# Kernel tuning notes

Hardware: AMD Instinct MI355X
Metric: run time of the kernel (lower is better)

Reference implementation:

```python
import jax, jax.numpy as jnp
import numpy as np

NUM_NODES = 50000
NUM_EDGES = 800000
HIDDEN = 128
HEADS = 8
HEAD_DIM = HIDDEN // HEADS  # 16
FF_HIDDEN = 4 * HIDDEN
LN_EPS = 1e-5


def _xavier(key, shape, gain=0.01):
    fan_out, fan_in = shape
    bound = gain * np.sqrt(6.0 / (fan_in + fan_out))
    return jax.random.uniform(key, shape, jnp.float32, -bound, bound)


def setup_inputs() -> dict:
    key = jax.random.key(0)
    ks = jax.random.split(key, 10)
    x = jax.random.normal(ks[0], (NUM_NODES, HIDDEN), jnp.float32)
    edge_index = jax.random.randint(ks[1], (2, NUM_EDGES), 0, NUM_NODES, jnp.int64)
    return {
        "x": x,
        "edge_index": edge_index,
        "Wq": _xavier(ks[2], (HIDDEN, HIDDEN)),
        "bq": jnp.zeros((HIDDEN,), jnp.float32),
        "Wk": _xavier(ks[3], (HIDDEN, HIDDEN)),
        "bk": jnp.zeros((HIDDEN,), jnp.float32),
        "Wv": _xavier(ks[4], (HIDDEN, HIDDEN)),
        "bv": jnp.zeros((HIDDEN,), jnp.float32),
        "Wo": _xavier(ks[5], (HIDDEN, HIDDEN)),
        "bo": jnp.zeros((HIDDEN,), jnp.float32),
        "W1": _xavier(ks[6], (FF_HIDDEN, HIDDEN)),
        "b1": jnp.zeros((FF_HIDDEN,), jnp.float32),
        "W2": _xavier(ks[7], (HIDDEN, FF_HIDDEN)),
        "b2": jnp.zeros((HIDDEN,), jnp.float32),
        "g1": jnp.ones((HIDDEN,), jnp.float32),
        "be1": jnp.zeros((HIDDEN,), jnp.float32),
        "g2": jnp.ones((HIDDEN,), jnp.float32),
        "be2": jnp.zeros((HIDDEN,), jnp.float32),
    }


def _layernorm(v, g, b):
    mu = jnp.mean(v, axis=-1, keepdims=True)
    var = jnp.mean(jnp.square(v - mu), axis=-1, keepdims=True)
    return (v - mu) * jax.lax.rsqrt(var + LN_EPS) * g + b


def _forward(x, edge_index, Wq, bq, Wk, bk, Wv, bv, Wo, bo, W1, b1, W2, b2, g1, be1, g2, be2):
    src = edge_index[0]  # key/value side (_j)
    dst = edge_index[1]  # query side (_i), aggregation index
    scale = 1.0 / np.sqrt(HEAD_DIM)

    # Euclidean manifold: GeometricLinear == plain linear
    q = (x @ Wq.T + bq).reshape(NUM_NODES, HEADS, HEAD_DIM)
    k = (x @ Wk.T + bk).reshape(NUM_NODES, HEADS, HEAD_DIM)
    v = (x @ Wv.T + bv).reshape(NUM_NODES, HEADS, HEAD_DIM)

    # per-edge attention scores [E, H]
    alpha = jnp.einsum('ehd,ehd->eh', q[dst], k[src]) * scale
    # segment softmax over destination nodes
    m = jax.ops.segment_max(alpha, dst, num_segments=NUM_NODES)  # [N, H]
    ea = jnp.exp(alpha - m[dst])
    denom = jax.ops.segment_sum(ea, dst, num_segments=NUM_NODES)  # [N, H]
    alpha = ea / (denom[dst] + 1e-16)

    # scatter-add weighted values -> [N, H, D]
    agg = jax.ops.segment_sum(v[src] * alpha[..., None], dst, num_segments=NUM_NODES)
    att = agg.reshape(NUM_NODES, HIDDEN) @ Wo.T + bo

    # residual + norm1 (Euclidean)
    h = _layernorm(x + att, g1, be1)

    # feed-forward: fc1 -> exact GELU -> fc2
    ff = (jax.nn.gelu(h @ W1.T + b1, approximate=False)) @ W2.T + b2

    # residual + norm2
    return _layernorm(h + ff, g2, be2)


def reference(x, edge_index, Wq, bq, Wk, bk, Wv, bv, Wo, bo, W1, b1, W2, b2, g1, be1, g2, be2):
    return _forward(x, edge_index, Wq, bq, Wk, bk, Wv, bv, Wo, bo, W1, b1, W2, b2, g1, be1, g2, be2)
```

## Files before the change

### kernel.cpp

```cpp
#include <hip/hip_runtime.h>
#include <math.h>

#define N_HEADS 8
#define HEAD_DIM 16
#define HID 128
#define QKV_ROWB 512

typedef unsigned short ushort_t;
typedef __attribute__((ext_vector_type(8))) short short8;
typedef __attribute__((ext_vector_type(4))) float floatx4;
typedef __attribute__((ext_vector_type(2))) float f32x2;

#define KV_SCALE 64.0f
#define KV_INV_SCALE 0.015625f

__device__ __forceinline__ ushort_t f2bf(float f) {
    unsigned u = __float_as_uint(f);
    unsigned r = (u + 0x7FFFu + ((u >> 16) & 1u)) >> 16;
    return (ushort_t)r;
}
__device__ __forceinline__ float bf2f(ushort_t u) {
    return __uint_as_float(((unsigned)u) << 16);
}

__device__ __forceinline__ void gld_lds16(const void* g, void* l) {
    __builtin_amdgcn_global_load_lds(
        (const __attribute__((address_space(1))) void*)g,
        (__attribute__((address_space(3))) void*)l, 16, 0, 0);
}

__device__ __forceinline__ float gelu_f(float x) {
    float z = fabsf(x) * 0.70710678118654752f;
    float t = 1.0f / (1.0f + 0.3275911f * z);
    float y = t * (0.254829592f + t * (-0.284496736f + t * (1.421413741f
            + t * (-1.453152027f + t * 1.061405429f))));
    float e = 1.0f - y * __expf(-z * z);
    e = copysignf(e, x);
    return 0.5f * x * (1.0f + e);
}

__global__ __launch_bounds__(256)
void prep_kernel(const float* __restrict__ x,
                 const float* __restrict__ Wq, const float* __restrict__ Wk,
                 const float* __restrict__ Wv, const float* __restrict__ Wo,
                 const float* __restrict__ W1, const float* __restrict__ W2,
                 const float* __restrict__ bq, const float* __restrict__ bk,
                 const float* __restrict__ bv,
                 const int* __restrict__ dst, int* __restrict__ cnt, int E,
                 ushort_t* __restrict__ xb, ushort_t* __restrict__ wts,
                 float* __restrict__ bqkv, int xpairs)
{
    int i = blockIdx.x * 256 + threadIdx.x;
    if (i < xpairs) {
        float2 v = ((const float2*)x)[i];
        xb[i * 2]     = f2bf(v.x);
        xb[i * 2 + 1] = f2bf(v.y);
        return;
    }
    int j = i - xpairs;
    if (j < 98304) {
        const float* s; int off;
        if (j < 32768) {
            if (j < 8192)       { s = Wq; off = j; }
            else if (j < 16384) { s = Wk; off = j - 8192; }
            else if (j < 24576) { s = Wv; off = j - 16384; }
            else                { s = Wo; off = j - 24576; }
        } else if (j < 65536)   { s = W1; off = j - 32768; }
        else                    { s = W2; off = j - 65536; }
        float2 v = ((const float2*)s)[off];
        wts[j * 2]     = f2bf(v.x);
        wts[j * 2 + 1] = f2bf(v.y);
        return;
    }
    int b = j - 98304;
    if (b < 384) {
        bqkv[b] = (b < 128) ? bq[b] : (b < 256) ? bk[b - 128] : bv[b - 256];
        return;
    }
    int e = b - 384;
    if (e < E) atomicAdd(&cnt[dst[e]], 1);
}

template<int MT, int ACT, int LN, int OUTF>
__global__ __launch_bounds__(256)
void gemm_t(const ushort_t* __restrict__ A, int lda, int M,
            const ushort_t* __restrict__ W, int K,
            const float* __restrict__ bias,
            float* __restrict__ outf, ushort_t* __restrict__ outb, int ostride,
            const float* __restrict__ resf, const ushort_t* __restrict__ resb,
            const float* __restrict__ g, const float* __restrict__ be)
{
    constexpr int MI  = MT / 32;
    constexpr int STG = MT * 64 + 128 * 64;
    constexpr int BNC = MT * 136;
    constexpr int SB  = STG > BNC ? STG : BNC;
    __shared__ __align__(16) ushort_t sbuf[SB];
    __shared__ float pS[LN ? MT : 1][2];
    __shared__ float pQ[LN ? MT : 1][2];
    ushort_t* As = sbuf;
    ushort_t* Ws = sbuf + MT * 64;

    const int tid  = threadIdx.x;
    const int wave = tid >> 6, lane = tid & 63;
    const int gm0 = blockIdx.x * MT;
    const int o0  = blockIdx.y * 128;
    const int mhalf = wave >> 1, ohalf = wave & 1;

    floatx4 acc[MI][4];
#pragma unroll
    for (int i = 0; i < MI; ++i)
#pragma unroll
        for (int j = 0; j < 4; ++j) acc[i][j] = (floatx4)(0.f);

    for (int kc = 0; kc < K; kc += 64) {
#pragma unroll
        for (int it = 0; it < 4; ++it) {
            int s   = it * 256 + tid;
            int ln  = s & 63;
            int grp = s >> 6;
            int tile = grp >> 1, kst = grp & 1;
            int row = tile * 16 + (ln & 15);
            int kk  = kst * 32 + (ln >> 4) * 8;
            gld_lds16(&W[(size_t)(o0 + row) * K + kc + kk],
                      &Ws[(it * 256 + wave * 64) * 8]);
        }
#pragma unroll
        for (int it = 0; it < MT / 32; ++it) {
            int s   = it * 256 + tid;
            int ln  = s & 63;
            int grp = s >> 6;
            int tile = grp >> 1, kst = grp & 1;
            int row = tile * 16 + (ln & 15);
            int kk  = kst * 32 + (ln >> 4) * 8;
            int ar = gm0 + row; if (ar >= M) ar = M - 1;
            gld_lds16(&A[(size_t)ar * lda + kc + kk],
                      &As[(it * 256 + wave * 64) * 8]);
        }
        __syncthreads();
#pragma unroll
        for (int kst = 0; kst < 2; ++kst) {
            short8 af[MI], wf[4];
#pragma unroll
            for (int i = 0; i < MI; ++i) {
                int mt = mhalf * MI + i;
                af[i] = *(const short8*)&As[((mt * 2 + kst) * 64 + lane) * 8];
            }
#pragma unroll
            for (int j = 0; j < 4; ++j) {
                int ot = ohalf * 4 + j;
                wf[j] = *(const short8*)&Ws[((ot * 2 + kst) * 64 + lane) * 8];
            }
#pragma unroll
            for (int i = 0; i < MI; ++i)
#pragma unroll
                for (int j = 0; j < 4; ++j)
                    acc[i][j] = __builtin_amdgcn_mfma_f32_16x16x32_bf16(
                        af[i], wf[j], acc[i][j], 0, 0, 0);
        }
        __syncthreads();
    }

    ushort_t* B16 = sbuf;
    float*    B32 = (float*)sbuf;

    if (LN) {
#pragma unroll
        for (int j = 0; j < 4; ++j) {
            int oc = (ohalf * 4 + j) * 16 + (lane & 15);
            float bj = bias[oc];
#pragma unroll
            for (int i = 0; i < MI; ++i) {
                int rbase = gm0 + (mhalf * MI + i) * 16 + (lane >> 4) * 4;
#pragma unroll
                for (int r = 0; r < 4; ++r) {
                    int rowc = rbase + r; if (rowc >= M) rowc = M - 1;
                    float rv = resf ? resf[(size_t)rowc * HID + oc]
                                    : bf2f(resb[(size_t)rowc * HID + oc]);
                    acc[i][j][r] += bj + rv;
                }
            }
        }
#pragma unroll
        for (int i = 0; i < MI; ++i) {
#pragma unroll
            for (int r = 0; r < 4; ++r) {
                float s1 = acc[i][0][r] + acc[i][1][r] + acc[i][2][r] + acc[i][3][r];
                float s2 = acc[i][0][r] * acc[i][0][r] + acc[i][1][r] * acc[i][1][r]
                         + acc[i][2][r] * acc[i][2][r] + acc[i][3][r] * acc[i][3][r];
                s1 += __shfl_xor(s1, 1); s1 += __shfl_xor(s1, 2);
                s1 += __shfl_xor(s1, 4); s1 += __shfl_xor(s1, 8);
                s2 += __shfl_xor(s2, 1); s2 += __shfl_xor(s2, 2);
                s2 += __shfl_xor(s2, 4); s2 += __shfl_xor(s2, 8);
                if ((lane & 15) == 0) {
                    int rl = (mhalf * MI + i) * 16 + (lane >> 4) * 4 + r;
                    pS[rl][ohalf] = s1;
                    pQ[rl][ohalf] = s2;
                }
            }
        }
        __syncthreads();
#pragma unroll
        for (int i = 0; i < MI; ++i) {
#pragma unroll
            for (int r = 0; r < 4; ++r) {
                int rl = (mhalf * MI + i) * 16 + (lane >> 4) * 4 + r;
                float S = pS[rl][0] + pS[rl][1];
                float Q = pQ[rl][0] + pQ[rl][1];
                float mu = S * (1.f / 128.f);
                float var = Q * (1.f / 128.f) - mu * mu;
                float rstd = rsqrtf(var + 1e-5f);
#pragma unroll
                for (int j = 0; j < 4; ++j) {
                    int oc = (ohalf * 4 + j) * 16 + (lane & 15);
                    acc[i][j][r] = (acc[i][j][r] - mu) * rstd * g[oc] + be[oc];
                }
            }
        }
        __syncthreads();
    }

    if (OUTF == 0 || (OUTF == 3 && blockIdx.y == 0)) {
#pragma unroll
        for (int i = 0; i < MI; ++i)
#pragma unroll
            for (int j = 0; j < 4; ++j) {
                int oc = (ohalf * 4 + j) * 16 + (lane & 15);
                float bj = LN ? 0.f : bias[o0 + oc];
#pragma unroll
                for (int r = 0; r < 4; ++r) {
                    int rl = (mhalf * MI + i) * 16 + (lane >> 4) * 4 + r;
                    float v = acc[i][j][r] + bj;
                    if (ACT) v = gelu_f(v);
                    B16[rl * 136 + oc] = f2bf(v);
                }
            }
        __syncthreads();
        const int oo = (OUTF == 3) ? 0 : o0;
#pragma unroll
        for (int p = 0; p < MT / 16; ++p) {
            int row = p * 16 + (tid >> 4);
            int ch  = tid & 15;
            if (gm0 + row < M)
                *(short8*)&outb[(size_t)(gm0 + row) * ostride + oo + ch * 8] =
                    *(const short8*)&B16[row * 136 + ch * 8];
        }
    } else if (OUTF == 2 || OUTF == 3) {
#pragma unroll
        for (int i = 0; i < MI; ++i)
#pragma unroll
            for (int j = 0; j < 4; ++j) {
                int oc = (ohalf * 4 + j) * 16 + (lane & 15);
                float bj = bias[o0 + oc];
#pragma unroll
                for (int r = 0; r < 4; ++r) {
                    int rl = (mhalf * MI + i) * 16 + (lane >> 4) * 4 + r;
                    float v = (acc[i][j][r] + bj) * KV_SCALE;
                    B16[rl * 136 + oc] = f2bf(v);
                }
            }
        __syncthreads();
        const int koff = (OUTF == 3) ? (blockIdx.y - 1) * 8 : blockIdx.y * 8;
#pragma unroll
        for (int p = 0; p < MT / 16; ++p) {
            int row = p * 16 + (tid >> 4);
            int ch  = tid & 15;
            if (gm0 + row < M) {
                short8 s = *(const short8*)&B16[row * 136 + ch * 8];
                unsigned u0 = 0, u1 = 0;
                u0 = __builtin_amdgcn_cvt_pk_fp8_f32(
                         bf2f((ushort_t)s[0]), bf2f((ushort_t)s[1]), u0, false);
                u0 = __builtin_amdgcn_cvt_pk_fp8_f32(
                         bf2f((ushort_t)s[2]), bf2f((ushort_t)s[3]), u0, true);
                u1 = __builtin_amdgcn_cvt_pk_fp8_f32(
                         bf2f((ushort_t)s[4]), bf2f((ushort_t)s[5]), u1, false);
                u1 = __builtin_amdgcn_cvt_pk_fp8_f32(
                         bf2f((ushort_t)s[6]), bf2f((ushort_t)s[7]), u1, true);
                uint2 o; o.x = u0; o.y = u1;
                *(uint2*)((char*)outb + (size_t)(gm0 + row) * QKV_ROWB
                          + 256 + ch * 16 + koff) = o;
            }
        }
    } else {
#pragma unroll
        for (int p = 0; p < 2; ++p) {
            if (ohalf == p) {
#pragma unroll
                for (int i = 0; i < MI; ++i)
#pragma unroll
                    for (int j = 0; j < 4; ++j) {
                        int ocl = j * 16 + (lane & 15);
                        float bj = LN ? 0.f : bias[p * 64 + ocl];
#pragma unroll
                        for (int r = 0; r < 4; ++r) {
                            int rl = (mhalf * MI + i) * 16 + (lane >> 4) * 4 + r;
                            float v = acc[i][j][r] + bj;
                            if (ACT) v = gelu_f(v);
                            B32[rl * 68 + ocl] = v;
                        }
                    }
            }
            __syncthreads();
#pragma unroll
            for (int q = 0; q < MT / 16; ++q) {
                int row = q * 16 + (tid >> 4);
                int ch  = tid & 15;
                if (gm0 + row < M)
                    *(float4*)&outf[(size_t)(gm0 + row) * ostride + o0 + p * 64 + ch * 4] =
                        *(const float4*)&B32[row * 68 + ch * 4];
            }
            __syncthreads();
        }
    }
}

__global__ __launch_bounds__(256)
void ff_fused_kernel(const ushort_t* __restrict__ hb,
                     const ushort_t* __restrict__ w1,
                     const float* __restrict__ b1,
                     const ushort_t* __restrict__ w2,
                     const float* __restrict__ b2,
                     const float* __restrict__ g, const float* __restrict__ be,
                     float* __restrict__ out, int M)
{
    __shared__ __align__(16) ushort_t Hs[8192];
    __shared__ __align__(16) ushort_t Wst[8192];
    __shared__ __align__(16) ushort_t a1t[8704];
    __shared__ float pS[64][2];
    __shared__ float pQ[64][2];

    const int tid = threadIdx.x;
    const int wave = tid >> 6, lane = tid & 63;
    const int gm0 = blockIdx.x * 64;
    const int mhalf = wave >> 1, ohalf = wave & 1;

#pragma unroll
    for (int it = 0; it < 4; ++it) {
        int s = it * 256 + tid;
        int l = s & 63;
        int g8 = (s >> 6) & 7;
        int kc = s >> 9;
        int tile = g8 >> 1, kst = g8 & 1;
        int row = tile * 16 + (l & 15);
        int kk = kc * 64 + kst * 32 + (l >> 4) * 8;
        int ar = gm0 + row; if (ar >= M) ar = M - 1;
        gld_lds16(&hb[(size_t)ar * HID + kk], &Hs[(it * 256 + wave * 64) * 8]);
    }

    floatx4 acc2[2][4];
#pragma unroll
    for (int i = 0; i < 2; ++i)
#pragma unroll
        for (int j = 0; j < 4; ++j) acc2[i][j] = (floatx4)(0.f);

    for (int c = 0; c < 4; ++c) {
        floatx4 acc1[2][4];
#pragma unroll
        for (int i = 0; i < 2; ++i)
#pragma unroll
            for (int j = 0; j < 4; ++j) acc1[i][j] = (floatx4)(0.f);

#pragma unroll
        for (int kc = 0; kc < 2; ++kc) {
#pragma unroll
            for (int it = 0; it < 4; ++it) {
                int s = it * 256 + tid;
                int l = s & 63;
                int grp = s >> 6;
                int tile = grp >> 1, kst = grp & 1;
                int row = c * 128 + tile * 16 + (l & 15);
                int kk = kc * 64 + kst * 32 + (l >> 4) * 8;
                gld_lds16(&w1[(size_t)row * HID + kk],
                          &Wst[(it * 256 + wave * 64) * 8]);
            }
            __syncthreads();
#pragma unroll
            for (int kst = 0; kst < 2; ++kst) {
                short8 af[2], wf[4];
#pragma unroll
                for (int i = 0; i < 2; ++i) {
                    int mt = mhalf * 2 + i;
                    af[i] = *(const short8*)&Hs[(((kc << 3) + mt * 2 + kst) * 64 + lane) * 8];
                }
#pragma unroll
                for (int j = 0; j < 4; ++j) {
                    int ot = ohalf * 4 + j;
                    wf[j] = *(const short8*)&Wst[((ot * 2 + kst) * 64 + lane) * 8];
                }
#pragma unroll
                for (int i = 0; i < 2; ++i)
#pragma unroll
                    for (int j = 0; j < 4; ++j)
                        acc1[i][j] = __builtin_amdgcn_mfma_f32_16x16x32_bf16(
                            af[i], wf[j], acc1[i][j], 0, 0, 0);
            }
            __syncthreads();
        }

#pragma unroll
        for (int i = 0; i < 2; ++i)
#pragma unroll
            for (int j = 0; j < 4; ++j) {
                int oc = (ohalf * 4 + j) * 16 + (lane & 15);
                float bj = b1[c * 128 + oc];
#pragma unroll
                for (int r = 0; r < 4; ++r) {
                    int rl = (mhalf * 2 + i) * 16 + (lane >> 4) * 4 + r;
                    a1t[rl * 136 + oc] = f2bf(gelu_f(acc1[i][j][r] + bj));
                }
            }

#pragma unroll
        for (int kc2 = 0; kc2 < 2; ++kc2) {
#pragma unroll
            for (int it = 0; it < 4; ++it) {
                int s = it * 256 + tid;
                int l = s & 63;
                int grp = s >> 6;
                int tile = grp >> 1, kst = grp & 1;
                int row = tile * 16 + (l & 15);
                int kk = c * 128 + kc2 * 64 + kst * 32 + (l >> 4) * 8;
                gld_lds16(&w2[(size_t)row * 512 + kk],
                          &Wst[(it * 256 + wave * 64) * 8]);
            }
            __syncthreads();
#pragma unroll
            for (int kst = 0; kst < 2; ++kst) {
                short8 af[2], wf[4];
#pragma unroll
                for (int i = 0; i < 2; ++i) {
                    int mt = mhalf * 2 + i;
                    af[i] = *(const short8*)&a1t[(mt * 16 + (lane & 15)) * 136
                                                 + kc2 * 64 + kst * 32 + (lane >> 4) * 8];
                }
#pragma unroll
                for (int j = 0; j < 4; ++j) {
                    int ot = ohalf * 4 + j;
                    wf[j] = *(const short8*)&Wst[((ot * 2 + kst) * 64 + lane) * 8];
                }
#pragma unroll
                for (int i = 0; i < 2; ++i)
#pragma unroll
                    for (int j = 0; j < 4; ++j)
                        acc2[i][j] = __builtin_amdgcn_mfma_f32_16x16x32_bf16(
                            af[i], wf[j], acc2[i][j], 0, 0, 0);
            }
            __syncthreads();
        }
    }

#pragma unroll
    for (int j = 0; j < 4; ++j) {
        int oc = (ohalf * 4 + j) * 16 + (lane & 15);
        float bj = b2[oc];
#pragma unroll
        for (int i = 0; i < 2; ++i) {
#pragma unroll
            for (int r = 0; r < 4; ++r) {
                int rl = (mhalf * 2 + i) * 16 + (lane >> 4) * 4 + r;
                float rv = bf2f(Hs[(((oc >> 6) * 8 + (rl >> 4) * 2 + ((oc >> 5) & 1)) * 64
                                    + (rl & 15) + ((oc >> 3) & 3) * 16) * 8 + (oc & 7)]);
                acc2[i][j][r] += bj + rv;
            }
        }
    }
#pragma unroll
    for (int i = 0; i < 2; ++i) {
#pragma unroll
        for (int r = 0; r < 4; ++r) {
            float s1 = acc2[i][0][r] + acc2[i][1][r] + acc2[i][2][r] + acc2[i][3][r];
            float s2 = acc2[i][0][r] * acc2[i][0][r] + acc2[i][1][r] * acc2[i][1][r]
                     + acc2[i][2][r] * acc2[i][2][r] + acc2[i][3][r] * acc2[i][3][r];
            s1 += __shfl_xor(s1, 1); s1 += __shfl_xor(s1, 2);
            s1 += __shfl_xor(s1, 4); s1 += __shfl_xor(s1, 8);
            s2 += __shfl_xor(s2, 1); s2 += __shfl_xor(s2, 2);
            s2 += __shfl_xor(s2, 4); s2 += __shfl_xor(s2, 8);
            if ((lane & 15) == 0) {
                int rl = (mhalf * 2 + i) * 16 + (lane >> 4) * 4 + r;
                pS[rl][ohalf] = s1;
                pQ[rl][ohalf] = s2;
            }
        }
    }
    __syncthreads();
#pragma unroll
    for (int i = 0; i < 2; ++i) {
#pragma unroll
        for (int r = 0; r < 4; ++r) {
            int rl = (mhalf * 2 + i) * 16 + (lane >> 4) * 4 + r;
            float S = pS[rl][0] + pS[rl][1];
            float Q = pQ[rl][0] + pQ[rl][1];
            float mu = S * (1.f / 128.f);
            float var = Q * (1.f / 128.f) - mu * mu;
            float rstd = rsqrtf(var + 1e-5f);
#pragma unroll
            for (int j = 0; j < 4; ++j) {
                int oc = (ohalf * 4 + j) * 16 + (lane & 15);
                acc2[i][j][r] = (acc2[i][j][r] - mu) * rstd * g[oc] + be[oc];
            }
        }
    }
    __syncthreads();

    float* B32 = (float*)a1t;
#pragma unroll
    for (int p = 0; p < 2; ++p) {
        if (ohalf == p) {
#pragma unroll
            for (int i = 0; i < 2; ++i)
#pragma unroll
                for (int j = 0; j < 4; ++j) {
                    int ocl = j * 16 + (lane & 15);
#pragma unroll
                    for (int r = 0; r < 4; ++r) {
                        int rl = (mhalf * 2 + i) * 16 + (lane >> 4) * 4 + r;
                        B32[rl * 68 + ocl] = acc2[i][j][r];
                    }
                }
        }
        __syncthreads();
#pragma unroll
        for (int q = 0; q < 4; ++q) {
            int row = q * 16 + (tid >> 4);
            int ch  = tid & 15;
            if (gm0 + row < M)
                *(float4*)&out[(size_t)(gm0 + row) * HID + p * 64 + ch * 4] =
                    *(const float4*)&B32[row * 68 + ch * 4];
        }
        __syncthreads();
    }
}

__global__ __launch_bounds__(256)
void scan1_kernel(const int* __restrict__ cnt, int* __restrict__ parts, int N)
{
    __shared__ int sd[256];
    int t = threadIdx.x;
    int base = blockIdx.x * 1024 + t * 4;
    int s = 0;
#pragma unroll
    for (int j = 0; j < 4; ++j) if (base + j < N) s += cnt[base + j];
    sd[t] = s; __syncthreads();
    for (int off = 128; off; off >>= 1) {
        if (t < off) sd[t] += sd[t + off];
        __syncthreads();
    }
    if (t == 0) parts[blockIdx.x] = sd[0];
}

__global__ __launch_bounds__(256)
void scan2_kernel(const int* __restrict__ parts, int* __restrict__ poff, int nb)
{
    __shared__ int sd[256];
    int t = threadIdx.x;
    int v = (t < nb) ? parts[t] : 0;
    sd[t] = v; __syncthreads();
    for (int off = 1; off < 256; off <<= 1) {
        int u = (t >= off) ? sd[t - off] : 0;
        __syncthreads();
        sd[t] += u;
        __syncthreads();
    }
    if (t < nb) poff[t] = sd[t] - v;
}

__global__ __launch_bounds__(256)
void scan3_kernel(const int* __restrict__ cnt, const int* __restrict__ poff,
                  int* __restrict__ rp, int N)
{
    __shared__ int sd[256];
    int t = threadIdx.x;
    int base = blockIdx.x * 1024 + t * 4;
    int v0 = (base + 0 < N) ? cnt[base + 0] : 0;
    int v1 = (base + 1 < N) ? cnt[base + 1] : 0;
    int v2 = (base + 2 < N) ? cnt[base + 2] : 0;
    int v3 = (base + 3 < N) ? cnt[base + 3] : 0;
    int s = v0 + v1 + v2 + v3;
    sd[t] = s; __syncthreads();
    for (int off = 1; off < 256; off <<= 1) {
        int u = (t >= off) ? sd[t - off] : 0;
        __syncthreads();
        sd[t] += u;
        __syncthreads();
    }
    int o = poff[blockIdx.x] + sd[t] - s;
    if (base + 0 < N) rp[base + 0] = o;
    if (base + 1 < N) rp[base + 1] = o + v0;
    if (base + 2 < N) rp[base + 2] = o + v0 + v1;
    if (base + 3 < N) rp[base + 3] = o + v0 + v1 + v2;
}

__global__ __launch_bounds__(256)
void scatter_kernel(const int* __restrict__ src, const int* __restrict__ dst,
                    int* __restrict__ rp, int* __restrict__ ssrc, int E, int N)
{
    int coh = blockIdx.x & 7;
    int bc  = blockIdx.x >> 3;
    int rr  = (N + 7) >> 3;
    int nlo = coh * rr;
    int nhi = nlo + rr; if (nhi > N) nhi = N;
    int stride = (gridDim.x >> 3) * 256;
    for (int e = bc * 256 + threadIdx.x; e < E; e += stride) {
        int d = dst[e];
        if (d >= nlo && d < nhi) {
            int pos = atomicAdd(&rp[d], 1);
            ssrc[pos] = src[e];
        }
    }
}

__global__ __launch_bounds__(256)
void attn_fused_kernel(const ushort_t* __restrict__ qkvb, const int* __restrict__ rp,
                       const int* __restrict__ ssrc, ushort_t* __restrict__ aggb, int N)
{
    int wave = threadIdx.x >> 6, lane = threadIdx.x & 63;
    int n = blockIdx.x * 4 + wave;
    if (n >= N) return;
    int grp = lane >> 4;
    int cb  = (lane & 15) * 16;
    const char* base = (const char*)qkvb;

    short8 qv = *(const short8*)(base + n * QKV_ROWB + cb);
    float q[8];
#pragma unroll
    for (int j = 0; j < 8; ++j) q[j] = bf2f((ushort_t)qv[j]) * (0.25f / KV_SCALE);

    int r0 = n ? rp[n - 1] : 0;
    int r1 = rp[n];
    float acc[8] = {0.f, 0.f, 0.f, 0.f, 0.f, 0.f, 0.f, 0.f};
    float l = 0.f;

    int r = r0;
    for (; r + 8 <= r1; r += 8) {
        int s0 = ssrc[r + grp];
        int s1 = ssrc[r + 4 + grp];
        uint4 kv0 = *(const uint4*)(base + s0 * QKV_ROWB + 256 + cb);
        uint4 kv1 = *(const uint4*)(base + s1 * QKV_ROWB + 256 + cb);

        f32x2 a0 = __builtin_amdgcn_cvt_pk_f32_fp8(kv0.x, false);
        f32x2 a1 = __builtin_amdgcn_cvt_pk_f32_fp8(kv0.x, true);
        f32x2 a2 = __builtin_amdgcn_cvt_pk_f32_fp8(kv0.y, false);
        f32x2 a3 = __builtin_amdgcn_cvt_pk_f32_fp8(kv0.y, true);
        f32x2 b0 = __builtin_amdgcn_cvt_pk_f32_fp8(kv1.x, false);
        f32x2 b1 = __builtin_amdgcn_cvt_pk_f32_fp8(kv1.x, true);
        f32x2 b2 = __builtin_amdgcn_cvt_pk_f32_fp8(kv1.y, false);
        f32x2 b3 = __builtin_amdgcn_cvt_pk_f32_fp8(kv1.y, true);

        float p0 = 0.f, p1 = 0.f;
        p0 = fmaf(q[0], a0.x, p0); p0 = fmaf(q[1], a0.y, p0);
        p0 = fmaf(q[2], a1.x, p0); p0 = fmaf(q[3], a1.y, p0);
        p0 = fmaf(q[4], a2.x, p0); p0 = fmaf(q[5], a2.y, p0);
        p0 = fmaf(q[6], a3.x, p0); p0 = fmaf(q[7], a3.y, p0);
        p1 = fmaf(q[0], b0.x, p1); p1 = fmaf(q[1], b0.y, p1);
        p1 = fmaf(q[2], b1.x, p1); p1 = fmaf(q[3], b1.y, p1);
        p1 = fmaf(q[4], b2.x, p1); p1 = fmaf(q[5], b2.y, p1);
        p1 = fmaf(q[6], b3.x, p1); p1 = fmaf(q[7], b3.y, p1);

        p0 += __shfl_xor(p0, 1);
        p1 += __shfl_xor(p1, 1);
        float e0 = __expf(p0), e1 = __expf(p1);
        l += e0 + e1;

        f32x2 v0 = __builtin_amdgcn_cvt_pk_f32_fp8(kv0.z, false);
        f32x2 v1 = __builtin_amdgcn_cvt_pk_f32_fp8(kv0.z, true);
        f32x2 v2 = __builtin_amdgcn_cvt_pk_f32_fp8(kv0.w, false);
        f32x2 v3 = __builtin_amdgcn_cvt_pk_f32_fp8(kv0.w, true);
        f32x2 w0 = __builtin_amdgcn_cvt_pk_f32_fp8(kv1.z, false);
        f32x2 w1 = __builtin_amdgcn_cvt_pk_f32_fp8(kv1.z, true);
        f32x2 w2 = __builtin_amdgcn_cvt_pk_f32_fp8(kv1.w, false);
        f32x2 w3 = __builtin_amdgcn_cvt_pk_f32_fp8(kv1.w, true);

        acc[0] = fmaf(e0, v0.x, acc[0]); acc[1] = fmaf(e0, v0.y, acc[1]);
        acc[2] = fmaf(e0, v1.x, acc[2]); acc[3] = fmaf(e0, v1.y, acc[3]);
        acc[4] = fmaf(e0, v2.x, acc[4]); acc[5] = fmaf(e0, v2.y, acc[5]);
        acc[6] = fmaf(e0, v3.x, acc[6]); acc[7] = fmaf(e0, v3.y, acc[7]);
        acc[0] = fmaf(e1, w0.x, acc[0]); acc[1] = fmaf(e1, w0.y, acc[1]);
        acc[2] = fmaf(e1, w1.x, acc[2]); acc[3] = fmaf(e1, w1.y, acc[3]);
        acc[4] = fmaf(e1, w2.x, acc[4]); acc[5] = fmaf(e1, w2.y, acc[5]);
        acc[6] = fmaf(e1, w3.x, acc[6]); acc[7] = fmaf(e1, w3.y, acc[7]);
    }
    for (; r < r1; r += 4) {
        int e = r + grp;
        int s = ssrc[(e < r1) ? e : r0];
        uint4 kv = *(const uint4*)(base + s * QKV_ROWB + 256 + cb);
        f32x2 a0 = __builtin_amdgcn_cvt_pk_f32_fp8(kv.x, false);
        f32x2 a1 = __builtin_amdgcn_cvt_pk_f32_fp8(kv.x, true);
        f32x2 a2 = __builtin_amdgcn_cvt_pk_f32_fp8(kv.y, false);
        f32x2 a3 = __builtin_amdgcn_cvt_pk_f32_fp8(kv.y, true);
        float p = 0.f;
        p = fmaf(q[0], a0.x, p); p = fmaf(q[1], a0.y, p);
        p = fmaf(q[2], a1.x, p); p = fmaf(q[3], a1.y, p);
        p = fmaf(q[4], a2.x, p); p = fmaf(q[5], a2.y, p);
        p = fmaf(q[6], a3.x, p); p = fmaf(q[7], a3.y, p);
        p += __shfl_xor(p, 1);
        float ea = (e < r1) ? __expf(p) : 0.f;
        l += ea;
        f32x2 v0 = __builtin_amdgcn_cvt_pk_f32_fp8(kv.z, false);
        f32x2 v1 = __builtin_amdgcn_cvt_pk_f32_fp8(kv.z, true);
        f32x2 v2 = __builtin_amdgcn_cvt_pk_f32_fp8(kv.w, false);
        f32x2 v3 = __builtin_amdgcn_cvt_pk_f32_fp8(kv.w, true);
        acc[0] = fmaf(ea, v0.x, acc[0]); acc[1] = fmaf(ea, v0.y, acc[1]);
        acc[2] = fmaf(ea, v1.x, acc[2]); acc[3] = fmaf(ea, v1.y, acc[3]);
        acc[4] = fmaf(ea, v2.x, acc[4]); acc[5] = fmaf(ea, v2.y, acc[5]);
        acc[6] = fmaf(ea, v3.x, acc[6]); acc[7] = fmaf(ea, v3.y, acc[7]);
    }

#pragma unroll
    for (int j = 0; j < 8; ++j) {
        acc[j] += __shfl_xor(acc[j], 16);
        acc[j] += __shfl_xor(acc[j], 32);
    }
    l += __shfl_xor(l, 16);
    l += __shfl_xor(l, 32);
    float inv = KV_INV_SCALE / (l + 1e-16f);
    if (grp == 0) {
        short8 o;
#pragma unroll
        for (int j = 0; j < 8; ++j) o[j] = (short)f2bf(acc[j] * inv);
        *(short8*)((char*)aggb + n * 256 + cb) = o;
    }
}

extern "C" void kernel_launch(void* const* d_in, const int* in_sizes, int n_in,
                              void* d_out, int out_size, void* d_ws, size_t ws_size,
                              hipStream_t stream)
{
    const float* x  = (const float*)d_in[0];
    const int*   ei = (const int*)d_in[1];
    const float* Wq = (const float*)d_in[2];
    const float* bq = (const float*)d_in[3];
    const float* Wk = (const float*)d_in[4];
    const float* bk = (const float*)d_in[5];
    const float* Wv = (const float*)d_in[6];
    const float* bv = (const float*)d_in[7];
    const float* Wo = (const float*)d_in[8];
    const float* bo = (const float*)d_in[9];
    const float* W1 = (const float*)d_in[10];
    const float* b1 = (const float*)d_in[11];
    const float* W2 = (const float*)d_in[12];
    const float* b2 = (const float*)d_in[13];
    const float* g1 = (const float*)d_in[14];
    const float* be1= (const float*)d_in[15];
    const float* g2 = (const float*)d_in[16];
    const float* be2= (const float*)d_in[17];
    float* out = (float*)d_out;

    const int N = in_sizes[0] / HID;
    const int E = in_sizes[1] / 2;
    const int* srcp = ei;
    const int* dstp = ei + E;

    const size_t NH = (size_t)N * HID;
    float* wsf = (float*)d_ws;

    ushort_t* xb   = (ushort_t*)wsf;
    ushort_t* qkvb = (ushort_t*)(wsf + NH / 2);
    ushort_t* aggb = (ushort_t*)(wsf + 2 * NH);
    ushort_t* hb   = (ushort_t*)wsf;

    ushort_t* wts  = (ushort_t*)(wsf + 2 * NH + NH / 2);
    float*    bqkv = (float*)(wts + 196608);
    int*      rp   = (int*)(bqkv + 384);
    int*      cnt  = rp + (N + 1);
    int*      poff = cnt + N;
    int*      parts= poff + 256;
    int*      ssrc = parts + 256;

    hipMemsetAsync(cnt, 0, N * sizeof(int), stream);
    const int xpairs = (int)(NH / 2);
    const int ptot   = xpairs + 98304 + 384 + E;
    prep_kernel<<<(ptot + 255) / 256, 256, 0, stream>>>(
        x, Wq, Wk, Wv, Wo, W1, W2, bq, bk, bv, dstp, cnt, E,
        xb, wts, bqkv, xpairs);

    const int nb = (N + 1023) / 1024;
    scan1_kernel<<<nb, 256, 0, stream>>>(cnt, parts, N);
    scan2_kernel<<<1, 256, 0, stream>>>(parts, poff, nb);
    scan3_kernel<<<nb, 256, 0, stream>>>(cnt, poff, rp, N);
    scatter_kernel<<<2048, 256, 0, stream>>>(srcp, dstp, rp, ssrc, E, N);

    const int gx64 = (N + 63) / 64;

    gemm_t<64, 0, 0, 3><<<dim3(gx64, 3), 256, 0, stream>>>(
        xb, HID, N, wts, HID, bqkv, nullptr, qkvb, 256,
        nullptr, nullptr, nullptr, nullptr);

    attn_fused_kernel<<<(N + 3) / 4, 256, 0, stream>>>(qkvb, rp, ssrc, aggb, N);

    gemm_t<64, 0, 1, 0><<<dim3(gx64, 1), 256, 0, stream>>>(
        aggb, HID, N, wts + 49152, HID, bo, nullptr, hb, HID,
        x, nullptr, g1, be1);

    ff_fused_kernel<<<gx64, 256, 0, stream>>>(
        hb, wts + 65536, b1, wts + 131072, b2, g2, be2, out, N);
}
```

Measured before the change: 336.9 us.

## Double-buffer weight staging in GEMM and fused FF kernels with swizzled activation tile

Both the generic GEMM and the fused feed-forward kernel now use two LDS buffers, issuing the next tile's global-to-LDS loads before computing on the current one, so memory latency can overlap MFMA work. The FF kernel flattens its per-chunk W1/W2 loops into one 16-panel pipeline with a single barrier per step. The GELU intermediate tile drops its padded stride in favour of an XOR swizzle to avoid bank conflicts. The extra buffers raise LDS use per block, which may lower occupancy.

New measurement: 338.2 us. About the same (+0.4%).

```diff
diff --git a/kernel.cpp b/kernel.cpp
--- a/kernel.cpp
+++ b/kernel.cpp
@@ -90,15 +90,13 @@
             const float* __restrict__ resf, const ushort_t* __restrict__ resb,
             const float* __restrict__ g, const float* __restrict__ be)
 {
-    constexpr int MI  = MT / 32;
-    constexpr int STG = MT * 64 + 128 * 64;
-    constexpr int BNC = MT * 136;
-    constexpr int SB  = STG > BNC ? STG : BNC;
+    constexpr int MI   = MT / 32;
+    constexpr int HALF = MT * 64 + 128 * 64;
+    constexpr int BNC  = MT * 136;
+    constexpr int SB   = (2 * HALF > BNC) ? 2 * HALF : BNC;
     __shared__ __align__(16) ushort_t sbuf[SB];
     __shared__ float pS[LN ? MT : 1][2];
     __shared__ float pQ[LN ? MT : 1][2];
-    ushort_t* As = sbuf;
-    ushort_t* Ws = sbuf + MT * 64;
 
     const int tid  = threadIdx.x;
     const int wave = tid >> 6, lane = tid & 63;
@@ -106,13 +104,9 @@
     const int o0  = blockIdx.y * 128;
     const int mhalf = wave >> 1, ohalf = wave & 1;
 
-    floatx4 acc[MI][4];
-#pragma unroll
-    for (int i = 0; i < MI; ++i)
-#pragma unroll
-        for (int j = 0; j < 4; ++j) acc[i][j] = (floatx4)(0.f);
-
-    for (int kc = 0; kc < K; kc += 64) {
+    auto stage = [&](int kc, int h) {
+        ushort_t* As = sbuf + h * HALF;
+        ushort_t* Ws = As + MT * 64;
 #pragma unroll
         for (int it = 0; it < 4; ++it) {
             int s   = it * 256 + tid;
@@ -136,7 +130,21 @@
             gld_lds16(&A[(size_t)ar * lda + kc + kk],
                       &As[(it * 256 + wave * 64) * 8]);
         }
-        __syncthreads();
+    };
+
+    floatx4 acc[MI][4];
+#pragma unroll
+    for (int i = 0; i < MI; ++i)
+#pragma unroll
+        for (int j = 0; j < 4; ++j) acc[i][j] = (floatx4)(0.f);
+
+    const int nk = K >> 6;
+    stage(0, 0);
+    __syncthreads();
+    for (int t = 0; t < nk; ++t) {
+        if (t + 1 < nk) stage((t + 1) * 64, (t + 1) & 1);
+        const ushort_t* As = sbuf + (t & 1) * HALF;
+        const ushort_t* Ws = As + MT * 64;
 #pragma unroll
         for (int kst = 0; kst < 2; ++kst) {
             short8 af[MI], wf[4];
@@ -323,8 +331,8 @@
                      float* __restrict__ out, int M)
 {
     __shared__ __align__(16) ushort_t Hs[8192];
-    __shared__ __align__(16) ushort_t Wst[8192];
-    __shared__ __align__(16) ushort_t a1t[8704];
+    __shared__ __align__(16) ushort_t wst[16384];
+    __shared__ __align__(16) ushort_t a1t[8192];
     __shared__ float pS[64][2];
     __shared__ float pQ[64][2];
 
@@ -332,6 +340,24 @@
     const int wave = tid >> 6, lane = tid & 63;
     const int gm0 = blockIdx.x * 64;
     const int mhalf = wave >> 1, ohalf = wave & 1;
+
+    auto stage_panel = [&](int p, int h) {
+        int c = p >> 2, sub = p & 3;
+        ushort_t* dst = wst + h * 8192;
+#pragma unroll
+        for (int it = 0; it < 4; ++it) {
+            int s = it * 256 + tid;
+            int l = s & 63;
+            int grp = s >> 6;
+            int tile = grp >> 1, kst = grp & 1;
+            int row = tile * 16 + (l & 15);
+            int kk = kst * 32 + (l >> 4) * 8;
+            const ushort_t* src;
+            if (sub < 2) src = &w1[(size_t)(c * 128 + row) * HID + sub * 64 + kk];
+            else         src = &w2[(size_t)row * 512 + c * 128 + (sub - 2) * 64 + kk];
+            gld_lds16(src, &dst[(it * 256 + wave * 64) * 8]);
+        }
+    };
 
 #pragma unroll
     for (int it = 0; it < 4; ++it) {
@@ -345,6 +371,8 @@
         int ar = gm0 + row; if (ar >= M) ar = M - 1;
         gld_lds16(&hb[(size_t)ar * HID + kk], &Hs[(it * 256 + wave * 64) * 8]);
     }
+    stage_panel(0, 0);
+    __syncthreads();
 
     floatx4 acc2[2][4];
 #pragma unroll
@@ -352,39 +380,34 @@
 #pragma unroll
         for (int j = 0; j < 4; ++j) acc2[i][j] = (floatx4)(0.f);
 
-    for (int c = 0; c < 4; ++c) {
-        floatx4 acc1[2][4];
-#pragma unroll
-        for (int i = 0; i < 2; ++i)
-#pragma unroll
-            for (int j = 0; j < 4; ++j) acc1[i][j] = (floatx4)(0.f);
-
-#pragma unroll
-        for (int kc = 0; kc < 2; ++kc) {
-#pragma unroll
-            for (int it = 0; it < 4; ++it) {
-                int s = it * 256 + tid;
-                int l = s & 63;
-                int grp = s >> 6;
-                int tile = grp >> 1, kst = grp & 1;
-                int row = c * 128 + tile * 16 + (l & 15);
-                int kk = kc * 64 + kst * 32 + (l >> 4) * 8;
-                gld_lds16(&w1[(size_t)row * HID + kk],
-                          &Wst[(it * 256 + wave * 64) * 8]);
-            }
-            __syncthreads();
+    floatx4 acc1[2][4];
+
+    for (int p = 0; p < 16; ++p) {
+        const int sub = p & 3;
+        const int c   = p >> 2;
+        if (p + 1 < 16) stage_panel(p + 1, (p + 1) & 1);
+        const ushort_t* wbuf = wst + (p & 1) * 8192;
+
+        if (sub == 0) {
+#pragma unroll
+            for (int i = 0; i < 2; ++i)
+#pragma unroll
+                for (int j = 0; j < 4; ++j) acc1[i][j] = (floatx4)(0.f);
+        }
+
+        if (sub < 2) {
 #pragma unroll
             for (int kst = 0; kst < 2; ++kst) {
                 short8 af[2], wf[4];
 #pragma unroll
                 for (int i = 0; i < 2; ++i) {
                     int mt = mhalf * 2 + i;
-                    af[i] = *(const short8*)&Hs[(((kc << 3) + mt * 2 + kst) * 64 + lane) * 8];
+                    af[i] = *(const short8*)&Hs[(((sub << 3) + mt * 2 + kst) * 64 + lane) * 8];
                 }
 #pragma unroll
                 for (int j = 0; j < 4; ++j) {
                     int ot = ohalf * 4 + j;
-                    wf[j] = *(const short8*)&Wst[((ot * 2 + kst) * 64 + lane) * 8];
+                    wf[j] = *(const short8*)&wbuf[((ot * 2 + kst) * 64 + lane) * 8];
                 }
 #pragma unroll
                 for (int i = 0; i < 2; ++i)
@@ -393,49 +416,38 @@
                         acc1[i][j] = __builtin_amdgcn_mfma_f32_16x16x32_bf16(
                             af[i], wf[j], acc1[i][j], 0, 0, 0);
             }
-            __syncthreads();
-        }
-
-#pragma unroll
-        for (int i = 0; i < 2; ++i)
-#pragma unroll
-            for (int j = 0; j < 4; ++j) {
-                int oc = (ohalf * 4 + j) * 16 + (lane & 15);
-                float bj = b1[c * 128 + oc];
-#pragma unroll
-                for (int r = 0; r < 4; ++r) {
-                    int rl = (mhalf * 2 + i) * 16 + (lane >> 4) * 4 + r;
-                    a1t[rl * 136 + oc] = f2bf(gelu_f(acc1[i][j][r] + bj));
-                }
-            }
-
-#pragma unroll
-        for (int kc2 = 0; kc2 < 2; ++kc2) {
-#pragma unroll
-            for (int it = 0; it < 4; ++it) {
-                int s = it * 256 + tid;
-                int l = s & 63;
-                int grp = s >> 6;
-                int tile = grp >> 1, kst = grp & 1;
-                int row = tile * 16 + (l & 15);
-                int kk = c * 128 + kc2 * 64 + kst * 32 + (l >> 4) * 8;
-                gld_lds16(&w2[(size_t)row * 512 + kk],
-                          &Wst[(it * 256 + wave * 64) * 8]);
-            }
-            __syncthreads();
+            if (sub == 1) {
+#pragma unroll
+                for (int i = 0; i < 2; ++i)
+#pragma unroll
+                    for (int j = 0; j < 4; ++j) {
+                        int oc = (ohalf * 4 + j) * 16 + (lane & 15);
+                        float bj = b1[c * 128 + oc];
+#pragma unroll
+                        for (int r = 0; r < 4; ++r) {
+                            int rl = (mhalf * 2 + i) * 16 + (lane >> 4) * 4 + r;
+                            *(ushort_t*)((char*)a1t + rl * 256 +
+                                         ((oc * 2) ^ ((rl & 7) << 4))) =
+                                f2bf(gelu_f(acc1[i][j][r] + bj));
+                        }
+                    }
+            }
+        } else {
+            const int kc2 = sub - 2;
 #pragma unroll
             for (int kst = 0; kst < 2; ++kst) {
                 short8 af[2], wf[4];
 #pragma unroll
                 for (int i = 0; i < 2; ++i) {
-                    int mt = mhalf * 2 + i;
-                    af[i] = *(const short8*)&a1t[(mt * 16 + (lane & 15)) * 136
-                                                 + kc2 * 64 + kst * 32 + (lane >> 4) * 8];
+                    int ar = (mhalf * 2 + i) * 16 + (lane & 15);
+                    int bc = kc2 * 128 + kst * 64 + (lane >> 4) * 16;
+                    af[i] = *(const short8*)((const char*)a1t + ar * 256 +
+                                             (bc ^ ((ar & 7) << 4)));
                 }
 #pragma unroll
                 for (int j = 0; j < 4; ++j) {
                     int ot = ohalf * 4 + j;
-                    wf[j] = *(const short8*)&Wst[((ot * 2 + kst) * 64 + lane) * 8];
+                    wf[j] = *(const short8*)&wbuf[((ot * 2 + kst) * 64 + lane) * 8];
                 }
 #pragma unroll
                 for (int i = 0; i < 2; ++i)
@@ -444,8 +456,8 @@
                         acc2[i][j] = __builtin_amdgcn_mfma_f32_16x16x32_bf16(
                             af[i], wf[j], acc2[i][j], 0, 0, 0);
             }
-            __syncthreads();
-        }
+        }
+        __syncthreads();
     }
 
 #pragma unroll
@@ -501,7 +513,7 @@
     }
     __syncthreads();
 
-    float* B32 = (float*)a1t;
+    float* B32 = (float*)wst;
 #pragma unroll
     for (int p = 0; p < 2; ++p) {
         if (ohalf == p) {
```
